# Optimization experiments

Measured on AMD Instinct MI355X. Metric: run time of the kernel, lower is better.

## Reference

```python
import jax, jax.numpy as jnp
import numpy as np

B, L, H, G = 16, 1024, 1024, 128


def setup_inputs() -> dict:
    key = jax.random.key(0)
    ks = jax.random.split(key, 6)
    s = 0.02
    return {
        "events": jax.random.normal(ks[0], (B, L, H), jnp.float32),
        "contexts": jax.random.normal(ks[1], (B, L - 1, H), jnp.float32),
        "Wzm": jax.random.normal(ks[2], (2 * H, G), jnp.float32) * s,
        "bzm": jnp.zeros((G,), jnp.float32),
        "Wzv": jax.random.normal(ks[3], (2 * H, G), jnp.float32) * s,
        "bzv": jnp.zeros((G,), jnp.float32),
        "Wqm": jax.random.normal(ks[4], (3 * H, G), jnp.float32) * s,
        "bqm": jnp.zeros((G,), jnp.float32),
        "Wqv": jax.random.normal(ks[5], (3 * H, G), jnp.float32) * s,
        "bqv": jnp.zeros((G,), jnp.float32),
    }


def reference(events, contexts, Wzm, bzm, Wzv, bzv, Wqm, bqm, Wqv, bqv):
    # adjacent event pairs: [B, L-1, 2H]
    ep = jnp.concatenate([events[:, :-1, :], events[:, 1:, :]], axis=-1)
    z_mean = ep @ Wzm + bzm          # [B, L-1, G]
    z_log_var = ep @ Wzv + bzv
    ce = jnp.concatenate([ep, contexts], axis=-1)  # [B, L-1, 3H]
    q_z_mean = ce @ Wqm + bqm
    q_z_log_var = ce @ Wqv + bqv
    # closed-form KL(p || q) for diagonal Gaussians, summed over G per (b, pair)
    kl = 0.5 * jnp.sum(
        q_z_log_var - z_log_var
        + (jnp.exp(z_log_var) + (z_mean - q_z_mean) ** 2) * jnp.exp(-q_z_log_var)
        - 1.0,
        axis=-1,
    )  # [B, L-1]
    kl_loss = jnp.mean(kl).reshape(1)  # sum over (b, pair) / (B * (L-1))
    return (z_mean, z_log_var, q_z_mean, q_z_log_var, kl_loss)
```

## Files before the change

kernel.cpp:

```cpp
#include <hip/hip_runtime.h>
#include <stdint.h>

typedef unsigned short u16;
typedef __attribute__((ext_vector_type(8))) short short8;
typedef __attribute__((ext_vector_type(4))) float f32x4;
typedef __attribute__((ext_vector_type(2))) uint32_t u32x2;

#define B_      16
#define L_      1024
#define H_      1024
#define G_      128
#define M_TOT   16368
#define K_TOT   3072
#define OUT_SEG 2095104
#define KL_IDX  (4*OUT_SEG)
#define KL_BLOCKS 2046

#define WS_WT_OFF    0
#define WS_BIAS_OFF  3145728
#define WS_PART_OFF  3147776

__device__ inline u16 f2bf(float f) {
    union { float f; uint32_t u; } x; x.f = f;
    uint32_t u = x.u;
    return (u16)((u + 0x7fffu + ((u >> 16) & 1u)) >> 16);
}

__device__ inline void gload16(const void* g, void* l) {
    __builtin_amdgcn_global_load_lds(
        (const __attribute__((address_space(1))) void*)g,
        (__attribute__((address_space(3))) void*)l, 16, 0, 0);
}

__global__ __launch_bounds__(256) void prep_kernel(
    const float* __restrict__ Wzm, const float* __restrict__ bzm,
    const float* __restrict__ Wzv, const float* __restrict__ bzv,
    const float* __restrict__ Wqm, const float* __restrict__ bqm,
    const float* __restrict__ Wqv, const float* __restrict__ bqv,
    u16* __restrict__ wt, float* __restrict__ bias)
{
    const int ng = blockIdx.x >> 2;
    const int kq = blockIdx.x & 3;
    const int n0 = ng * 8;
    const float* W; const float* bsrc; int g0; int kmax;
    if (n0 < 128)      { W = Wzm; bsrc = bzm; g0 = n0;       kmax = 2048; }
    else if (n0 < 256) { W = Wzv; bsrc = bzv; g0 = n0 - 128; kmax = 2048; }
    else if (n0 < 384) { W = Wqm; bsrc = bqm; g0 = n0 - 256; kmax = 3072; }
    else               { W = Wqv; bsrc = bqv; g0 = n0 - 384; kmax = 3072; }
    const int tid = threadIdx.x;
    if (kq == 0 && tid < 8) bias[n0 + tid] = bsrc[g0 + tid];

    __shared__ float lt[8][260];
    const int go = tid & 7;
    const int kk = tid >> 3;
    const int nn = tid >> 5;
    const int kc = (tid & 31) * 8;

    for (int i = 0; i < 3; ++i) {
        int kbase = kq * 768 + i * 256;
        __syncthreads();
        #pragma unroll
        for (int kk2 = 0; kk2 < 8; ++kk2) {
            int k = kbase + kk2 * 32 + kk;
            float v = (k < kmax) ? W[(size_t)k * G_ + g0 + go] : 0.0f;
            lt[go][kk2 * 32 + kk] = v;
        }
        __syncthreads();
        union { short8 s; u16 u[8]; } o;
        #pragma unroll
        for (int j = 0; j < 8; ++j) o.u[j] = f2bf(lt[nn][kc + j]);
        *(short8*)&wt[(size_t)(n0 + nn) * K_TOT + kbase + kc] = o.s;
    }
}

__global__ __launch_bounds__(512, 2) void gemm_kernel(
    const float* __restrict__ events, const float* __restrict__ contexts,
    const u16* __restrict__ wt, const float* __restrict__ bias,
    float* __restrict__ out)
{
    __shared__ u16 Ab[2][128 * 64];
    __shared__ u16 Bs[2][128 * 64];

    const int tid = threadIdx.x;
    const int bid = blockIdx.x;
    const int xx  = bid & 7;
    const int jj  = bid >> 3;
    const int nb  = jj & 3;
    const int mp  = (jj >> 2) * 8 + xx;
    const int m0  = mp * 128;

    const int lane = tid & 63;
    const int w    = tid >> 6;
    const int wm   = (w >> 2) * 64;
    const int wn   = (w & 3) * 32;
    const int lr   = lane & 15;
    const int kg   = lane >> 4;

    const int r = tid >> 2;
    const int q = tid & 3;
    int m = m0 + r; if (m > M_TOT - 1) m = M_TOT - 1;
    int bb = m / 1023;
    int tt = m - bb * 1023;
    const float* paE = events   + ((size_t)(bb * L_ + tt)) * H_;
    const float* paC = contexts + ((size_t)(bb * (L_ - 1) + tt)) * H_;
    int aw[4];
    #pragma unroll
    for (int j = 0; j < 4; ++j)
        aw[j] = r * 64 + (((2 * j + (q >> 1)) ^ (r & 7)) << 3) + (q & 1) * 4;

    const u16* bS[2];
    #pragma unroll
    for (int it = 0; it < 2; ++it) {
        int c  = it * 512 + tid;
        int v  = c >> 3;
        int cs = (c & 7) ^ (v & 7);
        bS[it] = wt + (size_t)(nb * 128 + v) * K_TOT + cs * 8;
    }

    int aoff[4][2], boff[2][2];
    #pragma unroll
    for (int i = 0; i < 4; ++i) {
        int row = wm + i * 16 + lr;
        #pragma unroll
        for (int ks = 0; ks < 2; ++ks)
            aoff[i][ks] = row * 64 + (((ks * 4 + kg) ^ (row & 7)) << 3);
    }
    #pragma unroll
    for (int j = 0; j < 2; ++j) {
        int nn = wn + j * 16 + lr;
        #pragma unroll
        for (int ks = 0; ks < 2; ++ks)
            boff[j][ks] = nn * 64 + (((ks * 4 + kg) ^ (nn & 7)) << 3);
    }

    f32x4 acc[4][2];
    #pragma unroll
    for (int i = 0; i < 4; ++i)
        #pragma unroll
        for (int j = 0; j < 2; ++j)
            acc[i][j] = (f32x4){0.f, 0.f, 0.f, 0.f};

    auto stageB = [&](int buf, int kt) {
        int k0 = kt * 64;
        gload16(bS[0] + k0, &Bs[buf][tid * 8]);
        gload16(bS[1] + k0, &Bs[buf][(512 + tid) * 8]);
    };
    auto compute = [&](int buf) {
        #pragma unroll
        for (int ks = 0; ks < 2; ++ks) {
            short8 a[4], bf[2];
            #pragma unroll
            for (int i = 0; i < 4; ++i)
                a[i] = *(const short8*)&Ab[buf][aoff[i][ks]];
            #pragma unroll
            for (int j = 0; j < 2; ++j)
                bf[j] = *(const short8*)&Bs[buf][boff[j][ks]];
            __builtin_amdgcn_s_setprio(1);
            #pragma unroll
            for (int i = 0; i < 4; ++i)
                #pragma unroll
                for (int j = 0; j < 2; ++j)
                    acc[i][j] = __builtin_amdgcn_mfma_f32_16x16x32_bf16(
                        a[i], bf[j], acc[i][j], 0, 0, 0);
            __builtin_amdgcn_s_setprio(0);
        }
    };

    f32x4 P0, P1, P2, P3;
    f32x4 Q0, Q1, Q2, Q3;

#define LOADA(p, KT)                                                           \
    {                                                                          \
        int k0_ = (KT) * 64;                                                   \
        int rg_ = (KT) >> 4;                                                   \
        int kq_ = (k0_ & 1023) + q * 4;                                        \
        const float* s_ = (rg_ == 0) ? paE : (rg_ == 1 ? (paE + H_) : paC);    \
        s_ += kq_;                                                             \
        p##0 = *(const f32x4*)(s_ +  0);                                       \
        p##1 = *(const f32x4*)(s_ + 16);                                       \
        p##2 = *(const f32x4*)(s_ + 32);                                       \
        p##3 = *(const f32x4*)(s_ + 48);                                       \
    }
#define CVT1(p, J, BUF)                                                        \
    {                                                                          \
        uint32_t lo_, hi_;                                                     \
        asm("v_cvt_pk_bf16_f32 %0, %1, %2" : "=v"(lo_) : "v"(p##J[0]), "v"(p##J[1])); \
        asm("v_cvt_pk_bf16_f32 %0, %1, %2" : "=v"(hi_) : "v"(p##J[2]), "v"(p##J[3])); \
        *(u32x2*)&Ab[BUF][aw[J]] = (u32x2){lo_, hi_};                          \
    }
#define CVTW(p, BUF)  CVT1(p, 0, BUF) CVT1(p, 1, BUF) CVT1(p, 2, BUF) CVT1(p, 3, BUF)

#define WAITV(N)                                                               \
    asm volatile("s_waitcnt vmcnt(" #N ")" ::: "memory");                      \
    __builtin_amdgcn_sched_barrier(0);
#define LGKM0                                                                  \
    asm volatile("s_waitcnt lgkmcnt(0)" ::: "memory");                         \
    __builtin_amdgcn_sched_barrier(0);
#define BAR __builtin_amdgcn_s_barrier()

    LOADA(P, 0);
    stageB(0, 0);
    WAITV(2);
    CVTW(P, 0);
    LOADA(Q, 1);
    LGKM0;

    for (int t = 0; t < 46; t += 2) {
        LOADA(P, t + 2);
        stageB(1, t + 1);
        WAITV(6); BAR;
        compute(0);
        CVTW(Q, 1);
        LGKM0; BAR;
        LOADA(Q, t + 3);
        stageB(0, t + 2);
        WAITV(6); BAR;
        compute(1);
        CVTW(P, 0);
        LGKM0; BAR;
    }
    stageB(1, 47);
    WAITV(2); BAR;
    compute(0);
    CVTW(Q, 1);
    LGKM0; BAR;
    WAITV(0); BAR;
    compute(1);

#undef LOADA
#undef CVT1
#undef CVTW
#undef WAITV
#undef LGKM0
#undef BAR

    const float* bptr = bias + nb * 128;
    float* obase = out + (size_t)nb * OUT_SEG;
    #pragma unroll
    for (int i = 0; i < 4; ++i) {
        int mloc = wm + i * 16 + kg * 4;
        #pragma unroll
        for (int j = 0; j < 2; ++j) {
            int g = wn + j * 16 + lr;
            float bv = bptr[g];
            #pragma unroll
            for (int rr = 0; rr < 4; ++rr) {
                int mo = m0 + mloc + rr;
                if (mo < M_TOT) obase[(size_t)mo * G_ + g] = acc[i][j][rr] + bv;
            }
        }
    }
}

__global__ __launch_bounds__(256) void kl_kernel(const float* __restrict__ out,
                                                 float* __restrict__ partial)
{
    int row  = blockIdx.x * 8 + (threadIdx.x >> 5);
    int col  = (threadIdx.x & 31) * 4;
    const float* zm  = out;
    const float* zlv = out + OUT_SEG;
    const float* qm  = out + (size_t)2 * OUT_SEG;
    const float* qlv = out + (size_t)3 * OUT_SEG;
    size_t base = (size_t)row * G_ + col;
    f32x4 a = *(const f32x4*)&zm[base];
    f32x4 b = *(const f32x4*)&zlv[base];
    f32x4 c = *(const f32x4*)&qm[base];
    f32x4 d = *(const f32x4*)&qlv[base];
    float s = 0.f;
    #pragma unroll
    for (int e = 0; e < 4; ++e) {
        float diff = a[e] - c[e];
        s += d[e] - b[e] + (__expf(b[e]) + diff * diff) * __expf(-d[e]) - 1.0f;
    }
    #pragma unroll
    for (int off = 32; off > 0; off >>= 1)
        s += __shfl_down(s, off);
    __shared__ float pw[4];
    int wid  = threadIdx.x >> 6;
    int lane = threadIdx.x & 63;
    if (lane == 0) pw[wid] = s;
    __syncthreads();
    if (threadIdx.x == 0)
        partial[blockIdx.x] = pw[0] + pw[1] + pw[2] + pw[3];
}

__global__ __launch_bounds__(256) void kl_final(const float* __restrict__ partial,
                                                float* __restrict__ out)
{
    float s = 0.f;
    for (int i = threadIdx.x; i < KL_BLOCKS; i += 256) s += partial[i];
    #pragma unroll
    for (int off = 32; off > 0; off >>= 1)
        s += __shfl_down(s, off);
    __shared__ float pw[4];
    int wid = threadIdx.x >> 6;
    int lane = threadIdx.x & 63;
    if (lane == 0) pw[wid] = s;
    __syncthreads();
    if (threadIdx.x == 0)
        out[KL_IDX] = 0.5f * (pw[0] + pw[1] + pw[2] + pw[3]) / (float)M_TOT;
}

extern "C" void kernel_launch(void* const* d_in, const int* in_sizes, int n_in,
                              void* d_out, int out_size, void* d_ws, size_t ws_size,
                              hipStream_t stream)
{
    const float* events   = (const float*)d_in[0];
    const float* contexts = (const float*)d_in[1];
    const float* Wzm = (const float*)d_in[2];
    const float* bzm = (const float*)d_in[3];
    const float* Wzv = (const float*)d_in[4];
    const float* bzv = (const float*)d_in[5];
    const float* Wqm = (const float*)d_in[6];
    const float* bqm = (const float*)d_in[7];
    const float* Wqv = (const float*)d_in[8];
    const float* bqv = (const float*)d_in[9];
    float* out = (float*)d_out;

    u16*   wt      = (u16*)((char*)d_ws + WS_WT_OFF);
    float* bias    = (float*)((char*)d_ws + WS_BIAS_OFF);
    float* partial = (float*)((char*)d_ws + WS_PART_OFF);

    prep_kernel<<<256, 256, 0, stream>>>(Wzm, bzm, Wzv, bzv, Wqm, bqm, Wqv, bqv,
                                         wt, bias);
    gemm_kernel<<<512, 512, 0, stream>>>(events, contexts, wt, bias, out);
    kl_kernel<<<KL_BLOCKS, 256, 0, stream>>>(out, partial);
    kl_final<<<1, 256, 0, stream>>>(partial, out);
}
```

Baseline: 94.47 us.

## Triple-buffer B tiles to use one barrier per K step

Adds a third shared-memory buffer for the B (weight) tile and restructures the main loop into a rotating three-stage schedule. Each K step now has a single barrier instead of two, and B staging for step k+2 is issued after compute. This targets barrier and synchronisation stalls in the bf16 MFMA GEMM. In exchange it uses more LDS (an extra 16 KB per block), which could reduce occupancy at two blocks per CU, and the hand-rotated buffer indices add correctness risk.

New measurement: 108.6 us. 15.0% more time.

```diff
diff --git a/kernel.cpp b/kernel.cpp
--- a/kernel.cpp
+++ b/kernel.cpp
@@ -79,7 +79,7 @@
     float* __restrict__ out)
 {
     __shared__ u16 Ab[2][128 * 64];
-    __shared__ u16 Bs[2][128 * 64];
+    __shared__ u16 Bs[3][128 * 64];
 
     const int tid = threadIdx.x;
     const int bid = blockIdx.x;
@@ -145,16 +145,16 @@
         gload16(bS[0] + k0, &Bs[buf][tid * 8]);
         gload16(bS[1] + k0, &Bs[buf][(512 + tid) * 8]);
     };
-    auto compute = [&](int buf) {
+    auto compute = [&](int abuf, int bbuf) {
         #pragma unroll
         for (int ks = 0; ks < 2; ++ks) {
             short8 a[4], bf[2];
             #pragma unroll
             for (int i = 0; i < 4; ++i)
-                a[i] = *(const short8*)&Ab[buf][aoff[i][ks]];
+                a[i] = *(const short8*)&Ab[abuf][aoff[i][ks]];
             #pragma unroll
             for (int j = 0; j < 2; ++j)
-                bf[j] = *(const short8*)&Bs[buf][boff[j][ks]];
+                bf[j] = *(const short8*)&Bs[bbuf][boff[j][ks]];
             __builtin_amdgcn_s_setprio(1);
             #pragma unroll
             for (int i = 0; i < 4; ++i)
@@ -196,43 +196,49 @@
 #define LGKM0                                                                  \
     asm volatile("s_waitcnt lgkmcnt(0)" ::: "memory");                         \
     __builtin_amdgcn_sched_barrier(0);
-#define BAR __builtin_amdgcn_s_barrier()
+#define BARS                                                                   \
+    __builtin_amdgcn_s_barrier();                                              \
+    __builtin_amdgcn_sched_barrier(0);
+
+#define PHASE(KT, AC, BC, BS2, PL, PC)                                         \
+    LOADA(PL, (KT) + 2);                                                       \
+    WAITV(6); LGKM0; BARS;                                                     \
+    compute(AC, BC);                                                           \
+    stageB(BS2, (KT) + 2);                                                     \
+    CVTW(PC, (AC) ^ 1);
 
     LOADA(P, 0);
     stageB(0, 0);
     WAITV(2);
     CVTW(P, 0);
     LOADA(Q, 1);
-    LGKM0;
-
-    for (int t = 0; t < 46; t += 2) {
-        LOADA(P, t + 2);
-        stageB(1, t + 1);
-        WAITV(6); BAR;
-        compute(0);
-        CVTW(Q, 1);
-        LGKM0; BAR;
-        LOADA(Q, t + 3);
-        stageB(0, t + 2);
-        WAITV(6); BAR;
-        compute(1);
-        CVTW(P, 0);
-        LGKM0; BAR;
-    }
-    stageB(1, 47);
-    WAITV(2); BAR;
-    compute(0);
+    stageB(1, 1);
+
+    for (int t = 0; t < 42; t += 6) {
+        PHASE(t,     0, 0, 2, P, Q);
+        PHASE(t + 1, 1, 1, 0, Q, P);
+        PHASE(t + 2, 0, 2, 1, P, Q);
+        PHASE(t + 3, 1, 0, 2, Q, P);
+        PHASE(t + 4, 0, 1, 0, P, Q);
+        PHASE(t + 5, 1, 2, 1, Q, P);
+    }
+    PHASE(42, 0, 0, 2, P, Q);
+    PHASE(43, 1, 1, 0, Q, P);
+    PHASE(44, 0, 2, 1, P, Q);
+    PHASE(45, 1, 0, 2, Q, P);
+    WAITV(2); LGKM0; BARS;
+    compute(0, 1);
     CVTW(Q, 1);
-    LGKM0; BAR;
-    WAITV(0); BAR;
-    compute(1);
-
+    WAITV(0); LGKM0; BARS;
+    compute(1, 2);
+
+#undef PHASE
 #undef LOADA
 #undef CVT1
 #undef CVTW
 #undef WAITV
 #undef LGKM0
-#undef BAR
+#undef BARS
 
     const float* bptr = bias + nb * 128;
     float* obase = out + (size_t)nb * OUT_SEG;
```

## Switch GEMM operands from bf16 to fp8 with scaled weights

Applied to the files above, without the earlier changes.

Converts activations and pre-scaled weights to fp8 (e4m3) and uses the fp8 MFMA instruction instead of bf16. The weights are multiplied by 128 before quantisation and the result is rescaled in the epilogue. LDS tiles, swizzles and the B staging are reworked for 1-byte elements, so one global-to-LDS load per thread now covers B. This halves LDS and weight traffic and raises MFMA throughput, but adds quantisation error that may break tolerance, since the inputs are normal with outliers and the logvar outputs feed exp().

After: 90.48 us, median of 3. 4.2% less time.

```diff
diff --git a/kernel.cpp b/kernel.cpp
--- a/kernel.cpp
+++ b/kernel.cpp
@@ -1,6 +1,7 @@
 #include <hip/hip_runtime.h>
 #include <stdint.h>
 
+typedef unsigned char u8;
 typedef unsigned short u16;
 typedef __attribute__((ext_vector_type(8))) short short8;
 typedef __attribute__((ext_vector_type(4))) float f32x4;
@@ -15,21 +16,23 @@
 #define OUT_SEG 2095104
 #define KL_IDX  (4*OUT_SEG)
 #define KL_BLOCKS 2046
+#define WSCALE  128.0f
+#define WINV    0.0078125f
 
 #define WS_WT_OFF    0
-#define WS_BIAS_OFF  3145728
-#define WS_PART_OFF  3147776
-
-__device__ inline u16 f2bf(float f) {
-    union { float f; uint32_t u; } x; x.f = f;
-    uint32_t u = x.u;
-    return (u16)((u + 0x7fffu + ((u >> 16) & 1u)) >> 16);
-}
+#define WS_BIAS_OFF  1572864
+#define WS_PART_OFF  1574912
 
 __device__ inline void gload16(const void* g, void* l) {
     __builtin_amdgcn_global_load_lds(
         (const __attribute__((address_space(1))) void*)g,
         (__attribute__((address_space(3))) void*)l, 16, 0, 0);
+}
+
+__device__ inline uint32_t pk4fp8(float f0, float f1, float f2, float f3) {
+    uint32_t w = __builtin_amdgcn_cvt_pk_fp8_f32(f0, f1, 0, 0);
+    w = __builtin_amdgcn_cvt_pk_fp8_f32(f2, f3, w, 1);
+    return w;
 }
 
 __global__ __launch_bounds__(256) void prep_kernel(
@@ -37,7 +40,7 @@
     const float* __restrict__ Wzv, const float* __restrict__ bzv,
     const float* __restrict__ Wqm, const float* __restrict__ bqm,
     const float* __restrict__ Wqv, const float* __restrict__ bqv,
-    u16* __restrict__ wt, float* __restrict__ bias)
+    u8* __restrict__ wt, float* __restrict__ bias)
 {
     const int ng = blockIdx.x >> 2;
     const int kq = blockIdx.x & 3;
@@ -66,20 +69,21 @@
             lt[go][kk2 * 32 + kk] = v;
         }
         __syncthreads();
-        union { short8 s; u16 u[8]; } o;
-        #pragma unroll
-        for (int j = 0; j < 8; ++j) o.u[j] = f2bf(lt[nn][kc + j]);
-        *(short8*)&wt[(size_t)(n0 + nn) * K_TOT + kbase + kc] = o.s;
+        uint32_t u0 = pk4fp8(lt[nn][kc + 0] * WSCALE, lt[nn][kc + 1] * WSCALE,
+                             lt[nn][kc + 2] * WSCALE, lt[nn][kc + 3] * WSCALE);
+        uint32_t u1 = pk4fp8(lt[nn][kc + 4] * WSCALE, lt[nn][kc + 5] * WSCALE,
+                             lt[nn][kc + 6] * WSCALE, lt[nn][kc + 7] * WSCALE);
+        *(u32x2*)&wt[(size_t)(n0 + nn) * K_TOT + kbase + kc] = (u32x2){u0, u1};
     }
 }
 
 __global__ __launch_bounds__(512, 2) void gemm_kernel(
     const float* __restrict__ events, const float* __restrict__ contexts,
-    const u16* __restrict__ wt, const float* __restrict__ bias,
+    const u8* __restrict__ wt, const float* __restrict__ bias,
     float* __restrict__ out)
 {
-    __shared__ u16 Ab[2][128 * 64];
-    __shared__ u16 Bs[2][128 * 64];
+    __shared__ u8 Ab[2][128 * 64];
+    __shared__ u8 Bs[2][128 * 64];
 
     const int tid = threadIdx.x;
     const int bid = blockIdx.x;
@@ -106,31 +110,31 @@
     int aw[4];
     #pragma unroll
     for (int j = 0; j < 4; ++j)
-        aw[j] = r * 64 + (((2 * j + (q >> 1)) ^ (r & 7)) << 3) + (q & 1) * 4;
-
-    const u16* bS[2];
-    #pragma unroll
-    for (int it = 0; it < 2; ++it) {
-        int c  = it * 512 + tid;
-        int v  = c >> 3;
-        int cs = (c & 7) ^ (v & 7);
-        bS[it] = wt + (size_t)(nb * 128 + v) * K_TOT + cs * 8;
-    }
+        aw[j] = r * 64 + (((j ^ ((r >> 1) & 3))) << 4) + q * 4;
+
+    const int bv   = tid >> 2;
+    const int bc   = tid & 3;
+    const int bcs  = bc ^ ((bv >> 1) & 3);
+    const u8* bS = wt + (size_t)(nb * 128 + bv) * K_TOT + bcs * 16;
 
     int aoff[4][2], boff[2][2];
     #pragma unroll
     for (int i = 0; i < 4; ++i) {
         int row = wm + i * 16 + lr;
         #pragma unroll
-        for (int ks = 0; ks < 2; ++ks)
-            aoff[i][ks] = row * 64 + (((ks * 4 + kg) ^ (row & 7)) << 3);
+        for (int ks = 0; ks < 2; ++ks) {
+            int c16 = ks * 2 + (kg >> 1);
+            aoff[i][ks] = row * 64 + ((c16 ^ ((row >> 1) & 3)) << 4) + (kg & 1) * 8;
+        }
     }
     #pragma unroll
     for (int j = 0; j < 2; ++j) {
         int nn = wn + j * 16 + lr;
         #pragma unroll
-        for (int ks = 0; ks < 2; ++ks)
-            boff[j][ks] = nn * 64 + (((ks * 4 + kg) ^ (nn & 7)) << 3);
+        for (int ks = 0; ks < 2; ++ks) {
+            int c16 = ks * 2 + (kg >> 1);
+            boff[j][ks] = nn * 64 + ((c16 ^ ((nn >> 1) & 3)) << 4) + (kg & 1) * 8;
+        }
     }
 
     f32x4 acc[4][2];
@@ -141,26 +145,24 @@
             acc[i][j] = (f32x4){0.f, 0.f, 0.f, 0.f};
 
     auto stageB = [&](int buf, int kt) {
-        int k0 = kt * 64;
-        gload16(bS[0] + k0, &Bs[buf][tid * 8]);
-        gload16(bS[1] + k0, &Bs[buf][(512 + tid) * 8]);
+        gload16(bS + kt * 64, &Bs[buf][tid * 16]);
     };
     auto compute = [&](int buf) {
         #pragma unroll
         for (int ks = 0; ks < 2; ++ks) {
-            short8 a[4], bf[2];
+            long a[4], bf[2];
             #pragma unroll
             for (int i = 0; i < 4; ++i)
-                a[i] = *(const short8*)&Ab[buf][aoff[i][ks]];
+                a[i] = *(const long*)&Ab[buf][aoff[i][ks]];
             #pragma unroll
             for (int j = 0; j < 2; ++j)
-                bf[j] = *(const short8*)&Bs[buf][boff[j][ks]];
+                bf[j] = *(const long*)&Bs[buf][boff[j][ks]];
             __builtin_amdgcn_s_setprio(1);
             #pragma unroll
             for (int i = 0; i < 4; ++i)
                 #pragma unroll
                 for (int j = 0; j < 2; ++j)
-                    acc[i][j] = __builtin_amdgcn_mfma_f32_16x16x32_bf16(
+                    acc[i][j] = __builtin_amdgcn_mfma_f32_16x16x32_fp8_fp8(
                         a[i], bf[j], acc[i][j], 0, 0, 0);
             __builtin_amdgcn_s_setprio(0);
         }
@@ -183,10 +185,8 @@
     }
 #define CVT1(p, J, BUF)                                                        \
     {                                                                          \
-        uint32_t lo_, hi_;                                                     \
-        asm("v_cvt_pk_bf16_f32 %0, %1, %2" : "=v"(lo_) : "v"(p##J[0]), "v"(p##J[1])); \
-        asm("v_cvt_pk_bf16_f32 %0, %1, %2" : "=v"(hi_) : "v"(p##J[2]), "v"(p##J[3])); \
-        *(u32x2*)&Ab[BUF][aw[J]] = (u32x2){lo_, hi_};                          \
+        uint32_t w_ = pk4fp8(p##J[0], p##J[1], p##J[2], p##J[3]);              \
+        *(uint32_t*)&Ab[BUF][aw[J]] = w_;                                      \
     }
 #define CVTW(p, BUF)  CVT1(p, 0, BUF) CVT1(p, 1, BUF) CVT1(p, 2, BUF) CVT1(p, 3, BUF)
 
@@ -200,7 +200,7 @@
 
     LOADA(P, 0);
     stageB(0, 0);
-    WAITV(2);
+    WAITV(1);
     CVTW(P, 0);
     LOADA(Q, 1);
     LGKM0;
@@ -208,19 +208,19 @@
     for (int t = 0; t < 46; t += 2) {
         LOADA(P, t + 2);
         stageB(1, t + 1);
-        WAITV(6); BAR;
+        WAITV(5); BAR;
         compute(0);
         CVTW(Q, 1);
         LGKM0; BAR;
         LOADA(Q, t + 3);
         stageB(0, t + 2);
-        WAITV(6); BAR;
+        WAITV(5); BAR;
         compute(1);
         CVTW(P, 0);
         LGKM0; BAR;
     }
     stageB(1, 47);
-    WAITV(2); BAR;
+    WAITV(1); BAR;
     compute(0);
     CVTW(Q, 1);
     LGKM0; BAR;
@@ -242,11 +242,12 @@
         #pragma unroll
         for (int j = 0; j < 2; ++j) {
             int g = wn + j * 16 + lr;
-            float bv = bptr[g];
+            float bv2 = bptr[g];
             #pragma unroll
             for (int rr = 0; rr < 4; ++rr) {
                 int mo = m0 + mloc + rr;
-                if (mo < M_TOT) obase[(size_t)mo * G_ + g] = acc[i][j][rr] + bv;
+                if (mo < M_TOT)
+                    obase[(size_t)mo * G_ + g] = acc[i][j][rr] * WINV + bv2;
             }
         }
     }
@@ -317,7 +318,7 @@
     const float* bqv = (const float*)d_in[9];
     float* out = (float*)d_out;
 
-    u16*   wt      = (u16*)((char*)d_ws + WS_WT_OFF);
+    u8*    wt      = (u8*)((char*)d_ws + WS_WT_OFF);
     float* bias    = (float*)((char*)d_ws + WS_BIAS_OFF);
     float* partial = (float*)((char*)d_ws + WS_PART_OFF);
 
```
